# Kernel optimization log

Measured on AMD Instinct MI355X. Metric: run time of the kernel, lower is better.

## Reference

```python
import jax, jax.numpy as jnp
import numpy as np

silu = jax.nn.silu

B, N, E, H, T, L, A = 8, 20000, 40000, 128, 64, 4, 4


def setup_inputs() -> dict:
    key = jax.random.key(0)
    ks = jax.random.split(key, 20)
    s = 0.05
    w = lambda k, shape: jax.random.normal(k, shape, jnp.float32) * s
    return {
        "x": jax.random.normal(ks[0], (B, N, 3), jnp.float32),
        "t": jax.random.uniform(ks[1], (B,), jnp.float32) * 1000.0,
        "atom_types": jax.random.randint(ks[2], (N,), 0, A),
        "bond_indices": jax.random.randint(ks[3], (E, 2), 0, N),
        "emb_table": w(ks[4], (A, H)),
        "W_t1": w(ks[5], (T, H)), "b_t1": jnp.zeros((H,), jnp.float32),
        "W_t2": w(ks[6], (H, H)), "b_t2": jnp.zeros((H,), jnp.float32),
        "W_node": w(ks[7], (H, H)), "b_node": jnp.zeros((H,), jnp.float32),
        "Wm1": w(ks[8], (L, 2 * H + 1, H)), "bm1": jnp.zeros((L, H), jnp.float32),
        "Wm2": w(ks[9], (L, H, H)), "bm2": jnp.zeros((L, H), jnp.float32),
        "Wn1": w(ks[10], (L, 2 * H, H)), "bn1": jnp.zeros((L, H), jnp.float32),
        "Wn2": w(ks[11], (L, H, H)), "bn2": jnp.zeros((L, H), jnp.float32),
        "Wc1": w(ks[12], (L, H, H)), "bc1": jnp.zeros((L, H), jnp.float32),
        "Wc2": w(ks[13], (L, H, 1)) * 0.001,  # xavier gain=0.001 final coord layer
        "W_o1": w(ks[14], (H, H)), "b_o1": jnp.zeros((H,), jnp.float32),
        "W_o2": w(ks[15], (H, 3)), "b_o2": jnp.zeros((3,), jnp.float32),
    }


def reference(x, t, atom_types, bond_indices, emb_table,
              W_t1, b_t1, W_t2, b_t2, W_node, b_node,
              Wm1, bm1, Wm2, bm2, Wn1, bn1, Wn2, bn2, Wc1, bc1, Wc2,
              W_o1, b_o1, W_o2, b_o2):
    n_atoms = x.shape[1]
    src = bond_indices[:, 0]
    dst = bond_indices[:, 1]

    # sinusoidal time embedding -> time MLP
    half = W_t1.shape[0] // 2
    freq = jnp.exp(jnp.arange(half, dtype=jnp.float32) * (-np.log(10000.0) / (half - 1)))
    te = t[:, None] * freq[None, :]
    te = jnp.concatenate([jnp.sin(te), jnp.cos(te)], axis=-1)  # [B, T]
    t_emb = silu(te @ W_t1 + b_t1) @ W_t2 + b_t2  # [B, H]

    # node init: embedding -> linear -> + time emb
    h0 = emb_table[atom_types] @ W_node + b_node  # [N, H]
    h = h0[None, :, :] + t_emb[:, None, :]  # [B, N, H]

    # degree counts (src+dst incidence), clamped to >=1
    ones = jnp.ones((src.shape[0],), jnp.float32)
    counts = jnp.zeros((n_atoms,), jnp.float32).at[dst].add(ones).at[src].add(ones)
    counts = jnp.maximum(counts, 1.0)

    x_orig = x
    n_layers = Wm1.shape[0]
    for l in range(n_layers):
        h_src = h[:, src, :]
        h_dst = h[:, dst, :]
        coord_diff = x[:, dst, :] - x[:, src, :]  # [B, E, 3]
        dist = jnp.sqrt(jnp.sum(coord_diff * coord_diff, axis=-1, keepdims=True))
        msg_in = jnp.concatenate([h_src, h_dst, dist], axis=-1)  # [B, E, 2H+1]
        m = silu(msg_in @ Wm1[l] + bm1[l])
        m = silu(m @ Wm2[l] + bm2[l])  # [B, E, H]

        agg = jnp.zeros_like(h).at[:, dst, :].add(m).at[:, src, :].add(m)
        h_in = jnp.concatenate([h, agg], axis=-1)
        h = h + silu(h_in @ Wn1[l] + bn1[l]) @ Wn2[l] + bn2[l]

        cw = silu(m @ Wc1[l] + bc1[l]) @ Wc2[l]  # [B, E, 1]
        cdn = coord_diff / (dist + 1e-8)
        upd = cdn * cw
        coord_update = jnp.zeros_like(x).at[:, dst, :].add(upd).at[:, src, :].add(-upd)
        x = x + coord_update / counts[None, :, None]

    coord_change = x - x_orig
    noise_from_h = silu(h @ W_o1 + b_o1) @ W_o2 + b_o2
    return coord_change + noise_from_h
```

## Files before the change

### kernel.cpp

```cpp
#include <hip/hip_runtime.h>
#include <math.h>

#define B_ 8
#define N_ 20000
#define E_ 40000
#define H_ 128
#define L_ 4
#define A_ 4
#define TS 132
#define MRS 136
#define EPB 64
#define NPB 64

#define WFENCE __asm__ __volatile__("" ::: "memory")

typedef _Float16 f16x8 __attribute__((ext_vector_type(8)));
typedef _Float16 f16x4v __attribute__((ext_vector_type(4)));
typedef float f32x4 __attribute__((ext_vector_type(4)));

__device__ __forceinline__ float silu_f(float x) {
    return x * __builtin_amdgcn_rcpf(1.f + __expf(-x));
}


__global__ void k_zero(int* __restrict__ deg, int* __restrict__ cursor) {
    int i = blockIdx.x * 256 + threadIdx.x;
    if (i < N_) { deg[i] = 0; cursor[i] = 0; }
}

__global__ void k_deg(const int* __restrict__ bond, int* __restrict__ deg) {
    int e = blockIdx.x * 256 + threadIdx.x;
    if (e < E_) {
        atomicAdd(&deg[bond[2 * e]], 1);
        atomicAdd(&deg[bond[2 * e + 1]], 1);
    }
}

__global__ void k_scan(const int* __restrict__ deg, int* __restrict__ indptr) {
    __shared__ int sums[1024];
    const int CH = (N_ + 1023) / 1024;
    int t = threadIdx.x;
    int s0 = t * CH;
    int s1 = min(s0 + CH, N_);
    int s = 0;
    for (int i = s0; i < s1; ++i) s += deg[i];
    sums[t] = s;
    __syncthreads();
    for (int off = 1; off < 1024; off <<= 1) {
        int v = (t >= off) ? sums[t - off] : 0;
        __syncthreads();
        sums[t] += v;
        __syncthreads();
    }
    int base = (t > 0) ? sums[t - 1] : 0;
    int run = base;
    for (int i = s0; i < s1; ++i) { indptr[i] = run; run += deg[i]; }
    if (s1 == N_ && s0 < N_) indptr[N_] = run;
}

__global__ void k_fill(const int* __restrict__ bond, const int* __restrict__ indptr,
                       int* __restrict__ cursor, int* __restrict__ adj) {
    int e = blockIdx.x * 256 + threadIdx.x;
    if (e < E_) {
        int s = bond[2 * e], d = bond[2 * e + 1];
        int ps = indptr[s] + atomicAdd(&cursor[s], 1);
        adj[ps] = (e << 1);
        int pd = indptr[d] + atomicAdd(&cursor[d], 1);
        adj[pd] = (e << 1) | 1;
    }
}

__global__ void k_wprepL(const float* __restrict__ W, _Float16* __restrict__ Wf,
                         int K, int wstride) {
    int l = blockIdx.y;
    const float* Wl = W + (size_t)l * wstride;
    _Float16* Wfl = Wf + (size_t)l * K * 128;
    int idx = blockIdx.x * 256 + threadIdx.x;
    if (idx >= K * 128) return;
    int j = idx & 7, lane = (idx >> 3) & 63, nt = (idx >> 9) & 7, kt = idx >> 12;
    int k = kt * 32 + (lane >> 4) * 8 + j;
    int n = nt * 16 + (lane & 15);
    Wfl[idx] = (_Float16)Wl[k * 128 + n];
}

__global__ void k_temb(const float* __restrict__ tv,
                       const float* __restrict__ W1, const float* __restrict__ b1,
                       const float* __restrict__ W2, const float* __restrict__ b2,
                       float* __restrict__ t_emb) {
    __shared__ float te[64];
    __shared__ float h1[128];
    int b = blockIdx.x;
    int tid = threadIdx.x;
    float tval = tv[b];
    if (tid < 32) {
        float fr = __expf((float)tid * (-logf(10000.f) / 31.f));
        float a = tval * fr;
        te[tid] = sinf(a);
        te[tid + 32] = cosf(a);
    }
    __syncthreads();
    float acc = b1[tid];
    for (int k = 0; k < 64; ++k) acc += te[k] * W1[k * 128 + tid];
    h1[tid] = silu_f(acc);
    __syncthreads();
    float acc2 = b2[tid];
    for (int k = 0; k < 128; ++k) acc2 += h1[k] * W2[k * 128 + tid];
    t_emb[b * 128 + tid] = acc2;
}

__global__ void k_embproj(const float* __restrict__ emb, const float* __restrict__ W,
                          const float* __restrict__ bias, float* __restrict__ outp) {
    int tid = threadIdx.x;
    int a = tid >> 7, j = tid & 127;
    float acc = bias[j];
    for (int k = 0; k < 128; ++k) acc += emb[a * 128 + k] * W[k * 128 + j];
    outp[a * 128 + j] = acc;
}

__global__ void k_hinit(const int* __restrict__ at, const float* __restrict__ embp,
                        const float* __restrict__ temb, float* __restrict__ h,
                        _Float16* __restrict__ h16) {
    size_t idx4 = (size_t)blockIdx.x * 256 + threadIdx.x;
    size_t e0 = idx4 * 4;
    int j = (int)(e0 % H_);
    size_t bn = e0 / H_;
    int n = (int)(bn % N_);
    int b = (int)(bn / N_);
    int a = at[n];
    float4 ep = *(const float4*)(embp + a * H_ + j);
    float4 tv = *(const float4*)(temb + b * H_ + j);
    float4 r = make_float4(ep.x + tv.x, ep.y + tv.y, ep.z + tv.z, ep.w + tv.w);
    ((float4*)h)[idx4] = r;
    f16x4v o;
    o[0] = (_Float16)r.x; o[1] = (_Float16)r.y; o[2] = (_Float16)r.z; o[3] = (_Float16)r.w;
    *(f16x4v*)(h16 + e0) = o;
}

__global__ void k_xcopy(const float* __restrict__ x, float* __restrict__ xb) {
    int i = blockIdx.x * 256 + threadIdx.x;
    xb[i] = x[i];
}

template <int RS, int KT>
__device__ __forceinline__ void mfma_gemm(const _Float16* Asw, const _Float16* __restrict__ Wf,
                                          f32x4 (&acc)[8], int ml, int quad, int lane) {
    #pragma unroll
    for (int kt = 0; kt < KT; ++kt) {
        f16x8 a = *(const f16x8*)(Asw + ml * RS + kt * 32 + quad * 8);
        #pragma unroll
        for (int nt = 0; nt < 8; ++nt) {
            f16x8 b = *(const f16x8*)(Wf + (((kt * 8 + nt) * 64 + lane) * 8));
            acc[nt] = __builtin_amdgcn_mfma_f32_16x16x32_f16(a, b, acc[nt], 0, 0, 0);
        }
    }
}

template <int RS, int KT>
__device__ __forceinline__ void mfma_gemm2(const _Float16* Asw, const _Float16* __restrict__ Wf,
                                           f32x4 (&acc)[2][8], int ml, int quad, int lane) {
    #pragma unroll
    for (int kt = 0; kt < KT; ++kt) {
        f16x8 a0 = *(const f16x8*)(Asw + ml * RS + kt * 32 + quad * 8);
        f16x8 a1 = *(const f16x8*)(Asw + (16 + ml) * RS + kt * 32 + quad * 8);
        #pragma unroll
        for (int nt = 0; nt < 8; ++nt) {
            f16x8 b = *(const f16x8*)(Wf + (((kt * 8 + nt) * 64 + lane) * 8));
            acc[0][nt] = __builtin_amdgcn_mfma_f32_16x16x32_f16(a0, b, acc[0][nt], 0, 0, 0);
            acc[1][nt] = __builtin_amdgcn_mfma_f32_16x16x32_f16(a1, b, acc[1][nt], 0, 0, 0);
        }
    }
}

template <int STRIDE, int K>
__device__ __forceinline__ void gemm_t(const float* As, const float* __restrict__ W,
                                       float (&acc)[4][8], int r4, int c) {
    const float4* Wv = (const float4*)W;
    #pragma unroll 2
    for (int k = 0; k < K; k += 4) {
        float a[4][4];
        #pragma unroll
        for (int i = 0; i < 4; ++i)
            *(float4*)a[i] = *(const float4*)(As + (r4 + i) * STRIDE + k);
        #pragma unroll
        for (int kk = 0; kk < 4; ++kk) {
            float4 w0 = Wv[(k + kk) * 32 + c * 2];
            float4 w1 = Wv[(k + kk) * 32 + c * 2 + 1];
            #pragma unroll
            for (int i = 0; i < 4; ++i) {
                float av = a[i][kk];
                acc[i][0] += av * w0.x; acc[i][1] += av * w0.y;
                acc[i][2] += av * w0.z; acc[i][3] += av * w0.w;
                acc[i][4] += av * w1.x; acc[i][5] += av * w1.y;
                acc[i][6] += av * w1.z; acc[i][7] += av * w1.w;
            }
        }
    }
}

__device__ __forceinline__ void bias_init(float (&acc)[4][8], const float* __restrict__ bias, int c) {
    float4 b0 = ((const float4*)bias)[c * 2];
    float4 b1 = ((const float4*)bias)[c * 2 + 1];
    #pragma unroll
    for (int i = 0; i < 4; ++i) {
        acc[i][0] = b0.x; acc[i][1] = b0.y; acc[i][2] = b0.z; acc[i][3] = b0.w;
        acc[i][4] = b1.x; acc[i][5] = b1.y; acc[i][6] = b1.z; acc[i][7] = b1.w;
    }
}


__global__ __launch_bounds__(128, 4) void k_edge_mfma(
    const _Float16* __restrict__ h16, const float* __restrict__ xcur,
    const int* __restrict__ bond,
    const float* __restrict__ Wm1, const float* __restrict__ bm1,
    const _Float16* __restrict__ Wm1f,
    const float* __restrict__ bm2, const _Float16* __restrict__ Wm2f,
    const float* __restrict__ bc1, const _Float16* __restrict__ Wc1f,
    const float* __restrict__ Wc2,
    _Float16* __restrict__ m16, float* __restrict__ cw_out) {
    __shared__ _Float16 As[EPB * MRS];
    __shared__ float ds_s[EPB];
    int tid = threadIdx.x;
    int b = blockIdx.x & 7;
    int e0 = (blockIdx.x >> 3) * EPB;
    size_t be0 = (size_t)b * E_ + e0;

    int el = tid >> 1, q = tid & 1;
    int2 sd = ((const int2*)bond)[e0 + el];
    int s = sd.x, d = sd.y;
    if (q == 0) {
        const float* xs = xcur + ((size_t)b * N_ + s) * 3;
        const float* xd = xcur + ((size_t)b * N_ + d) * 3;
        float dx = xd[0] - xs[0], dy = xd[1] - xs[1], dz = xd[2] - xs[2];
        ds_s[el] = sqrtf(dx * dx + dy * dy + dz * dz);
    }
    {
        const _Float16* hs = h16 + ((size_t)b * N_ + s) * H_;
        #pragma unroll
        for (int j = 0; j < 8; ++j)
            *(f16x8*)(As + el * MRS + q * 64 + j * 8) = *(const f16x8*)(hs + q * 64 + j * 8);
    }
    WFENCE;

    int lane = tid & 63, w = tid >> 6;
    int ml = lane & 15, quad = lane >> 4;
    _Float16* Asw = As + w * 32 * MRS;
    const float* wd = Wm1 + 256 * H_;

    f32x4 acc[2][8];
    #pragma unroll
    for (int nt = 0; nt < 8; ++nt) {
        int col = nt * 16 + ml;
        float bb = bm1[col];
        float ww = wd[col];
        #pragma unroll
        for (int rt = 0; rt < 2; ++rt)
            #pragma unroll
            for (int r = 0; r < 4; ++r)
                acc[rt][nt][r] = bb + ds_s[w * 32 + rt * 16 + quad * 4 + r] * ww;
    }
    mfma_gemm2<MRS, 4>(Asw, Wm1f, acc, ml, quad, lane);
    WFENCE;
    {
        const _Float16* hd = h16 + ((size_t)b * N_ + d) * H_;
        #pragma unroll
        for (int j = 0; j < 8; ++j)
            *(f16x8*)(As + el * MRS + q * 64 + j * 8) = *(const f16x8*)(hd + q * 64 + j * 8);
    }
    WFENCE;
    mfma_gemm2<MRS, 4>(Asw, Wm1f + 4 * 8 * 64 * 8, acc, ml, quad, lane);
    WFENCE;
    #pragma unroll
    for (int rt = 0; rt < 2; ++rt)
        #pragma unroll
        for (int nt = 0; nt < 8; ++nt)
            #pragma unroll
            for (int r = 0; r < 4; ++r)
                Asw[(rt * 16 + quad * 4 + r) * MRS + nt * 16 + ml] = (_Float16)silu_f(acc[rt][nt][r]);
    WFENCE;

    #pragma unroll
    for (int nt = 0; nt < 8; ++nt) {
        float bb = bm2[nt * 16 + ml];
        #pragma unroll
        for (int rt = 0; rt < 2; ++rt)
            #pragma unroll
            for (int r = 0; r < 4; ++r) acc[rt][nt][r] = bb;
    }
    mfma_gemm2<MRS, 4>(Asw, Wm2f, acc, ml, quad, lane);
    WFENCE;
    #pragma unroll
    for (int rt = 0; rt < 2; ++rt)
        #pragma unroll
        for (int nt = 0; nt < 8; ++nt)
            #pragma unroll
            for (int r = 0; r < 4; ++r)
                Asw[(rt * 16 + quad * 4 + r) * MRS + nt * 16 + ml] = (_Float16)silu_f(acc[rt][nt][r]);
    WFENCE;
    #pragma unroll
    for (int j = 0; j < 8; ++j)
        *(f16x8*)(m16 + (be0 + el) * H_ + q * 64 + j * 8) =
            *(const f16x8*)(As + el * MRS + q * 64 + j * 8);

    #pragma unroll
    for (int nt = 0; nt < 8; ++nt) {
        float bb = bc1[nt * 16 + ml];
        #pragma unroll
        for (int rt = 0; rt < 2; ++rt)
            #pragma unroll
            for (int r = 0; r < 4; ++r) acc[rt][nt][r] = bb;
    }
    mfma_gemm2<MRS, 4>(Asw, Wc1f, acc, ml, quad, lane);
    float part[2][4] = {{0.f, 0.f, 0.f, 0.f}, {0.f, 0.f, 0.f, 0.f}};
    #pragma unroll
    for (int nt = 0; nt < 8; ++nt) {
        float wv = Wc2[nt * 16 + ml];
        #pragma unroll
        for (int rt = 0; rt < 2; ++rt)
            #pragma unroll
            for (int r = 0; r < 4; ++r) part[rt][r] += silu_f(acc[rt][nt][r]) * wv;
    }
    #pragma unroll
    for (int off = 1; off < 16; off <<= 1)
        #pragma unroll
        for (int rt = 0; rt < 2; ++rt)
            #pragma unroll
            for (int r = 0; r < 4; ++r) part[rt][r] += __shfl_xor(part[rt][r], off, 64);
    if (ml == 0) {
        #pragma unroll
        for (int rt = 0; rt < 2; ++rt)
            #pragma unroll
            for (int r = 0; r < 4; ++r)
                cw_out[be0 + w * 32 + rt * 16 + quad * 4 + r] = part[rt][r];
    }
}

__global__ void k_coord(const float* __restrict__ xcur, float* __restrict__ xnext,
                        const float* __restrict__ cw, const int* __restrict__ bond,
                        const int* __restrict__ indptr, const int* __restrict__ adj) {
    int idx = blockIdx.x * 256 + threadIdx.x;
    int b = idx / N_;
    int n = idx - b * N_;
    const float* xb = xcur + (size_t)b * N_ * 3;
    int p0 = indptr[n], p1 = indptr[n + 1];
    float ax = 0.f, ay = 0.f, az = 0.f;
    for (int p = p0; p < p1; ++p) {
        int a = adj[p];
        int e = a >> 1;
        float sgn = (a & 1) ? 1.f : -1.f;
        int s = bond[2 * e], d = bond[2 * e + 1];
        float dx = xb[d * 3 + 0] - xb[s * 3 + 0];
        float dy = xb[d * 3 + 1] - xb[s * 3 + 1];
        float dz = xb[d * 3 + 2] - xb[s * 3 + 2];
        float dist = sqrtf(dx * dx + dy * dy + dz * dz);
        float w = cw[(size_t)b * E_ + e] * sgn * __builtin_amdgcn_rcpf(dist + 1e-8f);
        ax += dx * w; ay += dy * w; az += dz * w;
    }
    float rcnt = __builtin_amdgcn_rcpf((float)max(p1 - p0, 1));
    xnext[(size_t)idx * 3 + 0] = xb[n * 3 + 0] + ax * rcnt;
    xnext[(size_t)idx * 3 + 1] = xb[n * 3 + 1] + ay * rcnt;
    xnext[(size_t)idx * 3 + 2] = xb[n * 3 + 2] + az * rcnt;
}

__global__ __launch_bounds__(256, 5) void k_node_mfma(
    float* __restrict__ h, _Float16* __restrict__ h16,
    const _Float16* __restrict__ m16,
    const int* __restrict__ indptr, const int* __restrict__ adj,
    const float* __restrict__ bn1, const _Float16* __restrict__ Wn1f,
    const float* __restrict__ bn2, const _Float16* __restrict__ Wn2f) {
    __shared__ _Float16 As[NPB * MRS];
    int tid = threadIdx.x;
    int el = tid >> 2, q = tid & 3;
    int be = blockIdx.x * NPB + el;
    int b = be / N_, n = be - b * N_;
    {
        const _Float16* hr = h16 + (size_t)be * H_;
        #pragma unroll
        for (int j = 0; j < 4; ++j)
            *(f16x8*)(As + el * MRS + q * 32 + j * 8) = *(const f16x8*)(hr + q * 32 + j * 8);
    }
    WFENCE;

    int lane = tid & 63, w = tid >> 6;
    int ml = lane & 15, quad = lane >> 4;
    _Float16* Asw = As + w * 16 * MRS;
    size_t be0 = (size_t)blockIdx.x * NPB;

    f32x4 acc[8];
    #pragma unroll
    for (int nt = 0; nt < 8; ++nt) {
        float bb = bn1[nt * 16 + ml];
        #pragma unroll
        for (int r = 0; r < 4; ++r) acc[nt][r] = bb;
    }
    mfma_gemm<MRS, 4>(Asw, Wn1f, acc, ml, quad, lane);
    WFENCE;
    {
        float ag[4][8];
        #pragma unroll
        for (int j = 0; j < 4; ++j)
            #pragma unroll
            for (int i = 0; i < 8; ++i) ag[j][i] = 0.f;
        int p0 = indptr[n], p1 = indptr[n + 1];
        for (int p = p0; p < p1; ++p) {
            int e = adj[p] >> 1;
            const _Float16* mp = m16 + ((size_t)b * E_ + e) * H_;
            #pragma unroll
            for (int j = 0; j < 4; ++j) {
                f16x8 v = *(const f16x8*)(mp + q * 32 + j * 8);
                #pragma unroll
                for (int i = 0; i < 8; ++i) ag[j][i] += (float)v[i];
            }
        }
        #pragma unroll
        for (int j = 0; j < 4; ++j) {
            f16x8 o;
            #pragma unroll
            for (int i = 0; i < 8; ++i) o[i] = (_Float16)ag[j][i];
            *(f16x8*)(As + el * MRS + q * 32 + j * 8) = o;
        }
    }
    WFENCE;
    mfma_gemm<MRS, 4>(Asw, Wn1f + 4 * 8 * 64 * 8, acc, ml, quad, lane);
    WFENCE;
    #pragma unroll
    for (int nt = 0; nt < 8; ++nt)
        #pragma unroll
        for (int r = 0; r < 4; ++r)
            Asw[(quad * 4 + r) * MRS + nt * 16 + ml] = (_Float16)silu_f(acc[nt][r]);
    WFENCE;
    f32x4 acc2[8];
    #pragma unroll
    for (int nt = 0; nt < 8; ++nt) {
        float bb = bn2[nt * 16 + ml];
        #pragma unroll
        for (int r = 0; r < 4; ++r) acc2[nt][r] = bb;
    }
    mfma_gemm<MRS, 4>(Asw, Wn2f, acc2, ml, quad, lane);
    #pragma unroll
    for (int nt = 0; nt < 8; ++nt)
        #pragma unroll
        for (int r = 0; r < 4; ++r) {
            int row = w * 16 + quad * 4 + r;
            size_t g = (size_t)(be0 + row) * H_ + nt * 16 + ml;
            float v = h[g] + acc2[nt][r];
            h[g] = v;
            h16[g] = (_Float16)v;
        }
}

__global__ __launch_bounds__(256) void k_out2(
    const float* __restrict__ h, const float* __restrict__ xfin, const float* __restrict__ xorig,
    const float* __restrict__ Wo1, const float* __restrict__ bo1,
    const float* __restrict__ Wo2, const float* __restrict__ bo2,
    float* __restrict__ out) {
    __shared__ float As[64 * TS];
    __shared__ float red[64 * 48];
    int tid = threadIdx.x;
    {
        int nl = tid >> 2, q = tid & 3;
        size_t row = (size_t)blockIdx.x * 64 + nl;
        const float4* hr = (const float4*)(h + row * H_);
        #pragma unroll
        for (int j = 0; j < 8; ++j) {
            int f4 = j * 4 + q;
            *(float4*)(As + nl * TS + f4 * 4) = hr[f4];
        }
    }
    __syncthreads();
    int r4 = (tid >> 4) * 4, c = tid & 15;
    float acc[4][8];
    bias_init(acc, bo1, c);
    gemm_t<TS, 128>(As, Wo1, acc, r4, c);
    #pragma unroll
    for (int i = 0; i < 4; ++i) {
        float p0 = 0.f, p1 = 0.f, p2 = 0.f;
        #pragma unroll
        for (int j = 0; j < 8; ++j) {
            float u = silu_f(acc[i][j]);
            int col = c * 8 + j;
            p0 += u * Wo2[col * 3 + 0];
            p1 += u * Wo2[col * 3 + 1];
            p2 += u * Wo2[col * 3 + 2];
        }
        red[(r4 + i) * 48 + c * 3 + 0] = p0;
        red[(r4 + i) * 48 + c * 3 + 1] = p1;
        red[(r4 + i) * 48 + c * 3 + 2] = p2;
    }
    __syncthreads();
    if (tid < 192) {
        int row = tid / 3, jj = tid - row * 3;
        float s = 0.f;
        #pragma unroll
        for (int cc = 0; cc < 16; ++cc) s += red[row * 48 + cc * 3 + jj];
        size_t grow = (size_t)blockIdx.x * 64 + row;
        out[grow * 3 + jj] = s + bo2[jj] + xfin[grow * 3 + jj] - xorig[grow * 3 + jj];
    }
}


extern "C" void kernel_launch(void* const* d_in, const int* in_sizes, int n_in,
                              void* d_out, int out_size, void* d_ws, size_t ws_size,
                              hipStream_t stream) {
    const float* x = (const float*)d_in[0];
    const float* t = (const float*)d_in[1];
    const int* atom_types = (const int*)d_in[2];
    const int* bond = (const int*)d_in[3];
    const float* emb_table = (const float*)d_in[4];
    const float* W_t1 = (const float*)d_in[5];
    const float* b_t1 = (const float*)d_in[6];
    const float* W_t2 = (const float*)d_in[7];
    const float* b_t2 = (const float*)d_in[8];
    const float* W_node = (const float*)d_in[9];
    const float* b_node = (const float*)d_in[10];
    const float* Wm1 = (const float*)d_in[11];
    const float* bm1 = (const float*)d_in[12];
    const float* Wm2 = (const float*)d_in[13];
    const float* bm2 = (const float*)d_in[14];
    const float* Wn1 = (const float*)d_in[15];
    const float* bn1 = (const float*)d_in[16];
    const float* Wn2 = (const float*)d_in[17];
    const float* bn2 = (const float*)d_in[18];
    const float* Wc1 = (const float*)d_in[19];
    const float* bc1 = (const float*)d_in[20];
    const float* Wc2 = (const float*)d_in[21];
    const float* W_o1 = (const float*)d_in[22];
    const float* b_o1 = (const float*)d_in[23];
    const float* W_o2 = (const float*)d_in[24];
    const float* b_o2 = (const float*)d_in[25];
    float* out = (float*)d_out;

    char* p = (char*)d_ws;
    auto alloc = [&](size_t bytes) -> void* {
        void* r = (void*)p;
        p += (bytes + 255) & ~(size_t)255;
        return r;
    };
    float* t_emb = (float*)alloc((size_t)B_ * H_ * 4);
    float* emb_proj = (float*)alloc((size_t)A_ * H_ * 4);
    int* deg = (int*)alloc((size_t)N_ * 4);
    int* indptr = (int*)alloc((size_t)(N_ + 1) * 4);
    int* cursor = (int*)alloc((size_t)N_ * 4);
    int* adj = (int*)alloc((size_t)2 * E_ * 4);
    float* xb0 = (float*)alloc((size_t)B_ * N_ * 3 * 4);
    float* xb1 = (float*)alloc((size_t)B_ * N_ * 3 * 4);
    float* cw = (float*)alloc((size_t)B_ * E_ * 4);
    float* h = (float*)alloc((size_t)B_ * N_ * H_ * 4);
    _Float16* h16 = (_Float16*)alloc((size_t)B_ * N_ * H_ * 2);
    _Float16* m16 = (_Float16*)alloc((size_t)B_ * E_ * H_ * 2);
    _Float16* Wm1f = (_Float16*)alloc((size_t)L_ * 256 * H_ * 2);
    _Float16* Wm2f = (_Float16*)alloc((size_t)L_ * H_ * H_ * 2);
    _Float16* Wc1f = (_Float16*)alloc((size_t)L_ * H_ * H_ * 2);
    _Float16* Wn1f = (_Float16*)alloc((size_t)L_ * 256 * H_ * 2);
    _Float16* Wn2f = (_Float16*)alloc((size_t)L_ * H_ * H_ * 2);

    k_zero<<<(N_ + 255) / 256, 256, 0, stream>>>(deg, cursor);
    k_deg<<<(E_ + 255) / 256, 256, 0, stream>>>(bond, deg);
    k_scan<<<1, 1024, 0, stream>>>(deg, indptr);
    k_fill<<<(E_ + 255) / 256, 256, 0, stream>>>(bond, indptr, cursor, adj);
    k_temb<<<B_, 128, 0, stream>>>(t, W_t1, b_t1, W_t2, b_t2, t_emb);
    k_embproj<<<1, 512, 0, stream>>>(emb_table, W_node, b_node, emb_proj);
    k_hinit<<<(B_ * N_ * H_ / 4) / 256, 256, 0, stream>>>(atom_types, emb_proj, t_emb, h, h16);
    k_xcopy<<<(B_ * N_ * 3) / 256, 256, 0, stream>>>(x, xb0);
    k_wprepL<<<dim3(128, L_), 256, 0, stream>>>(Wm1, Wm1f, 256, 257 * H_);
    k_wprepL<<<dim3(64, L_), 256, 0, stream>>>(Wm2, Wm2f, 128, H_ * H_);
    k_wprepL<<<dim3(64, L_), 256, 0, stream>>>(Wc1, Wc1f, 128, H_ * H_);
    k_wprepL<<<dim3(128, L_), 256, 0, stream>>>(Wn1, Wn1f, 256, 2 * H_ * H_);
    k_wprepL<<<dim3(64, L_), 256, 0, stream>>>(Wn2, Wn2f, 128, H_ * H_);

    float* xc = xb0;
    float* xn = xb1;
    for (int l = 0; l < L_; ++l) {
        k_edge_mfma<<<(B_ * E_) / EPB, 128, 0, stream>>>(
            h16, xc, bond,
            Wm1 + (size_t)l * 257 * H_, bm1 + l * H_, Wm1f + (size_t)l * 256 * H_,
            bm2 + l * H_, Wm2f + (size_t)l * H_ * H_,
            bc1 + l * H_, Wc1f + (size_t)l * H_ * H_,
            Wc2 + (size_t)l * H_, m16, cw);
        k_coord<<<(B_ * N_) / 256, 256, 0, stream>>>(xc, xn, cw, bond, indptr, adj);
        k_node_mfma<<<(B_ * N_) / NPB, 256, 0, stream>>>(
            h, h16, m16, indptr, adj,
            bn1 + l * H_, Wn1f + (size_t)l * 256 * H_,
            bn2 + l * H_, Wn2f + (size_t)l * H_ * H_);
        float* tmp = xc; xc = xn; xn = tmp;
    }
    k_out2<<<(B_ * N_) / 64, 256, 0, stream>>>(h, xc, x, W_o1, b_o1, W_o2, b_o2, out);
}
```

Measured before the change: 1.129 ms.

## Use four waves per edge block and prefetch src/dst rows into registers

The edge kernel now runs 256 threads per 64-edge block, so each wave handles 16 edge rows instead of 32 and holds half the accumulator registers (single-tile mfma_gemm instead of mfma_gemm2). Launch bounds rise to 256 threads with 5 blocks per CU to raise occupancy. Both the source and destination h rows are loaded into registers at kernel start, so the destination gather latency overlaps the first GEMM instead of stalling between the two halves. In exchange, each weight tile is reloaded by twice as many waves per edge, which adds weight-read traffic.

```diff
diff --git a/kernel.cpp b/kernel.cpp
--- a/kernel.cpp
+++ b/kernel.cpp
@@ -208,7 +208,7 @@
 }
 
 
-__global__ __launch_bounds__(128, 4) void k_edge_mfma(
+__global__ __launch_bounds__(256, 5) void k_edge_mfma(
     const _Float16* __restrict__ h16, const float* __restrict__ xcur,
     const int* __restrict__ bond,
     const float* __restrict__ Wm1, const float* __restrict__ bm1,
@@ -224,9 +224,20 @@
     int e0 = (blockIdx.x >> 3) * EPB;
     size_t be0 = (size_t)b * E_ + e0;
 
-    int el = tid >> 1, q = tid & 1;
+    int el = tid >> 2, q = tid & 3;
     int2 sd = ((const int2*)bond)[e0 + el];
     int s = sd.x, d = sd.y;
+
+    const _Float16* hs = h16 + ((size_t)b * N_ + s) * H_ + q * 32;
+    f16x8 ps0 = *(const f16x8*)(hs);
+    f16x8 ps1 = *(const f16x8*)(hs + 8);
+    f16x8 ps2 = *(const f16x8*)(hs + 16);
+    f16x8 ps3 = *(const f16x8*)(hs + 24);
+    const _Float16* hd = h16 + ((size_t)b * N_ + d) * H_ + q * 32;
+    f16x8 pd0 = *(const f16x8*)(hd);
+    f16x8 pd1 = *(const f16x8*)(hd + 8);
+    f16x8 pd2 = *(const f16x8*)(hd + 16);
+    f16x8 pd3 = *(const f16x8*)(hd + 24);
     if (q == 0) {
         const float* xs = xcur + ((size_t)b * N_ + s) * 3;
         const float* xd = xcur + ((size_t)b * N_ + d) * 3;
@@ -234,103 +245,87 @@
         ds_s[el] = sqrtf(dx * dx + dy * dy + dz * dz);
     }
     {
-        const _Float16* hs = h16 + ((size_t)b * N_ + s) * H_;
-        #pragma unroll
-        for (int j = 0; j < 8; ++j)
-            *(f16x8*)(As + el * MRS + q * 64 + j * 8) = *(const f16x8*)(hs + q * 64 + j * 8);
+        _Float16* ap = As + el * MRS + q * 32;
+        *(f16x8*)(ap) = ps0; *(f16x8*)(ap + 8) = ps1;
+        *(f16x8*)(ap + 16) = ps2; *(f16x8*)(ap + 24) = ps3;
     }
     WFENCE;
 
     int lane = tid & 63, w = tid >> 6;
     int ml = lane & 15, quad = lane >> 4;
-    _Float16* Asw = As + w * 32 * MRS;
+    _Float16* Asw = As + w * 16 * MRS;
     const float* wd = Wm1 + 256 * H_;
 
-    f32x4 acc[2][8];
+    float dl[4];
+    #pragma unroll
+    for (int r = 0; r < 4; ++r) dl[r] = ds_s[w * 16 + quad * 4 + r];
+    f32x4 acc[8];
     #pragma unroll
     for (int nt = 0; nt < 8; ++nt) {
         int col = nt * 16 + ml;
         float bb = bm1[col];
         float ww = wd[col];
         #pragma unroll
-        for (int rt = 0; rt < 2; ++rt)
-            #pragma unroll
-            for (int r = 0; r < 4; ++r)
-                acc[rt][nt][r] = bb + ds_s[w * 32 + rt * 16 + quad * 4 + r] * ww;
-    }
-    mfma_gemm2<MRS, 4>(Asw, Wm1f, acc, ml, quad, lane);
+        for (int r = 0; r < 4; ++r) acc[nt][r] = bb + dl[r] * ww;
+    }
+    mfma_gemm<MRS, 4>(Asw, Wm1f, acc, ml, quad, lane);
     WFENCE;
     {
-        const _Float16* hd = h16 + ((size_t)b * N_ + d) * H_;
-        #pragma unroll
-        for (int j = 0; j < 8; ++j)
-            *(f16x8*)(As + el * MRS + q * 64 + j * 8) = *(const f16x8*)(hd + q * 64 + j * 8);
-    }
-    WFENCE;
-    mfma_gemm2<MRS, 4>(Asw, Wm1f + 4 * 8 * 64 * 8, acc, ml, quad, lane);
-    WFENCE;
-    #pragma unroll
-    for (int rt = 0; rt < 2; ++rt)
-        #pragma unroll
-        for (int nt = 0; nt < 8; ++nt)
-            #pragma unroll
-            for (int r = 0; r < 4; ++r)
-                Asw[(rt * 16 + quad * 4 + r) * MRS + nt * 16 + ml] = (_Float16)silu_f(acc[rt][nt][r]);
+        _Float16* ap = As + el * MRS + q * 32;
+        *(f16x8*)(ap) = pd0; *(f16x8*)(ap + 8) = pd1;
+        *(f16x8*)(ap + 16) = pd2; *(f16x8*)(ap + 24) = pd3;
+    }
+    WFENCE;
+    mfma_gemm<MRS, 4>(Asw, Wm1f + 4 * 8 * 64 * 8, acc, ml, quad, lane);
+    WFENCE;
+    #pragma unroll
+    for (int nt = 0; nt < 8; ++nt)
+        #pragma unroll
+        for (int r = 0; r < 4; ++r)
+            Asw[(quad * 4 + r) * MRS + nt * 16 + ml] = (_Float16)silu_f(acc[nt][r]);
     WFENCE;
 
     #pragma unroll
     for (int nt = 0; nt < 8; ++nt) {
         float bb = bm2[nt * 16 + ml];
         #pragma unroll
-        for (int rt = 0; rt < 2; ++rt)
-            #pragma unroll
-            for (int r = 0; r < 4; ++r) acc[rt][nt][r] = bb;
-    }
-    mfma_gemm2<MRS, 4>(Asw, Wm2f, acc, ml, quad, lane);
-    WFENCE;
-    #pragma unroll
-    for (int rt = 0; rt < 2; ++rt)
-        #pragma unroll
-        for (int nt = 0; nt < 8; ++nt)
-            #pragma unroll
-            for (int r = 0; r < 4; ++r)
-                Asw[(rt * 16 + quad * 4 + r) * MRS + nt * 16 + ml] = (_Float16)silu_f(acc[rt][nt][r]);
-    WFENCE;
-    #pragma unroll
-    for (int j = 0; j < 8; ++j)
-        *(f16x8*)(m16 + (be0 + el) * H_ + q * 64 + j * 8) =
-            *(const f16x8*)(As + el * MRS + q * 64 + j * 8);
+        for (int r = 0; r < 4; ++r) acc[nt][r] = bb;
+    }
+    mfma_gemm<MRS, 4>(Asw, Wm2f, acc, ml, quad, lane);
+    WFENCE;
+    #pragma unroll
+    for (int nt = 0; nt < 8; ++nt)
+        #pragma unroll
+        for (int r = 0; r < 4; ++r)
+            Asw[(quad * 4 + r) * MRS + nt * 16 + ml] = (_Float16)silu_f(acc[nt][r]);
+    WFENCE;
+    #pragma unroll
+    for (int j = 0; j < 4; ++j)
+        *(f16x8*)(m16 + (be0 + el) * H_ + q * 32 + j * 8) =
+            *(const f16x8*)(As + el * MRS + q * 32 + j * 8);
 
     #pragma unroll
     for (int nt = 0; nt < 8; ++nt) {
         float bb = bc1[nt * 16 + ml];
         #pragma unroll
-        for (int rt = 0; rt < 2; ++rt)
-            #pragma unroll
-            for (int r = 0; r < 4; ++r) acc[rt][nt][r] = bb;
-    }
-    mfma_gemm2<MRS, 4>(Asw, Wc1f, acc, ml, quad, lane);
-    float part[2][4] = {{0.f, 0.f, 0.f, 0.f}, {0.f, 0.f, 0.f, 0.f}};
+        for (int r = 0; r < 4; ++r) acc[nt][r] = bb;
+    }
+    mfma_gemm<MRS, 4>(Asw, Wc1f, acc, ml, quad, lane);
+    float part[4] = {0.f, 0.f, 0.f, 0.f};
     #pragma unroll
     for (int nt = 0; nt < 8; ++nt) {
         float wv = Wc2[nt * 16 + ml];
         #pragma unroll
-        for (int rt = 0; rt < 2; ++rt)
-            #pragma unroll
-            for (int r = 0; r < 4; ++r) part[rt][r] += silu_f(acc[rt][nt][r]) * wv;
+        for (int r = 0; r < 4; ++r) part[r] += silu_f(acc[nt][r]) * wv;
     }
     #pragma unroll
     for (int off = 1; off < 16; off <<= 1)
         #pragma unroll
-        for (int rt = 0; rt < 2; ++rt)
-            #pragma unroll
-            for (int r = 0; r < 4; ++r) part[rt][r] += __shfl_xor(part[rt][r], off, 64);
+        for (int r = 0; r < 4; ++r) part[r] += __shfl_xor(part[r], off, 64);
     if (ml == 0) {
         #pragma unroll
-        for (int rt = 0; rt < 2; ++rt)
-            #pragma unroll
-            for (int r = 0; r < 4; ++r)
-                cw_out[be0 + w * 32 + rt * 16 + quad * 4 + r] = part[rt][r];
+        for (int r = 0; r < 4; ++r)
+            cw_out[be0 + w * 16 + quad * 4 + r] = part[r];
     }
 }
 
@@ -570,7 +565,7 @@
     float* xc = xb0;
     float* xn = xb1;
     for (int l = 0; l < L_; ++l) {
-        k_edge_mfma<<<(B_ * E_) / EPB, 128, 0, stream>>>(
+        k_edge_mfma<<<(B_ * E_) / EPB, 256, 0, stream>>>(
             h16, xc, bond,
             Wm1 + (size_t)l * 257 * H_, bm1 + l * H_, Wm1f + (size_t)l * 256 * H_,
             bm2 + l * H_, Wm2f + (size_t)l * H_ * H_,
```

Measured after the change: 1.148 ms. No clear change (+1.6%).

## Double tile size, prefetch weight fragments, and swizzle blocks across XCDs

Applied to the files above, without the earlier changes.

Edge and node kernels now process 128 rows per block with 256 threads, and each wave computes two 16-row MFMA tiles so every weight fragment load is reused twice. A new GEMM helper double-buffers the B-operand weight fragments in registers, loading k-step kt+1 while the MFMAs for step kt run. Block indices are remapped so consecutive tiles land on the same XCD, which should improve L2 locality, and the edge kernel now overlaps the gather loads with the distance computation. The larger register footprint lowers the occupancy hint and could limit latency hiding.

```diff
diff --git a/kernel.cpp b/kernel.cpp
--- a/kernel.cpp
+++ b/kernel.cpp
@@ -9,8 +9,8 @@
 #define A_ 4
 #define TS 132
 #define MRS 136
-#define EPB 64
-#define NPB 64
+#define EPB 128
+#define NPB 128
 
 #define WFENCE __asm__ __volatile__("" ::: "memory")
 
@@ -20,6 +20,12 @@
 
 __device__ __forceinline__ float silu_f(float x) {
     return x * __builtin_amdgcn_rcpf(1.f + __expf(-x));
+}
+
+__device__ __forceinline__ int xcd_swz(int bid, int nwg) {
+    int q = nwg >> 3, r = nwg & 7;
+    int x = bid & 7, i = bid >> 3;
+    return (x < r ? x * (q + 1) : r * (q + 1) + (x - r) * q) + i;
 }
 
 
@@ -141,32 +147,26 @@
     xb[i] = x[i];
 }
 
-template <int RS, int KT>
-__device__ __forceinline__ void mfma_gemm(const _Float16* Asw, const _Float16* __restrict__ Wf,
-                                          f32x4 (&acc)[8], int ml, int quad, int lane) {
-    #pragma unroll
-    for (int kt = 0; kt < KT; ++kt) {
-        f16x8 a = *(const f16x8*)(Asw + ml * RS + kt * 32 + quad * 8);
-        #pragma unroll
-        for (int nt = 0; nt < 8; ++nt) {
-            f16x8 b = *(const f16x8*)(Wf + (((kt * 8 + nt) * 64 + lane) * 8));
-            acc[nt] = __builtin_amdgcn_mfma_f32_16x16x32_f16(a, b, acc[nt], 0, 0, 0);
-        }
-    }
-}
-
-template <int RS, int KT>
-__device__ __forceinline__ void mfma_gemm2(const _Float16* Asw, const _Float16* __restrict__ Wf,
-                                           f32x4 (&acc)[2][8], int ml, int quad, int lane) {
-    #pragma unroll
-    for (int kt = 0; kt < KT; ++kt) {
+template <int RS>
+__device__ __forceinline__ void mfma_gemm2p(const _Float16* Asw, const _Float16* __restrict__ Wf,
+                                            f32x4 (&acc)[2][8], int ml, int quad, int lane) {
+    const _Float16* wp = Wf + lane * 8;
+    f16x8 bb[2][8];
+    #pragma unroll
+    for (int nt = 0; nt < 8; ++nt) bb[0][nt] = *(const f16x8*)(wp + nt * 512);
+    #pragma unroll
+    for (int kt = 0; kt < 4; ++kt) {
+        if (kt < 3) {
+            #pragma unroll
+            for (int nt = 0; nt < 8; ++nt)
+                bb[(kt + 1) & 1][nt] = *(const f16x8*)(wp + ((kt + 1) * 8 + nt) * 512);
+        }
         f16x8 a0 = *(const f16x8*)(Asw + ml * RS + kt * 32 + quad * 8);
         f16x8 a1 = *(const f16x8*)(Asw + (16 + ml) * RS + kt * 32 + quad * 8);
         #pragma unroll
         for (int nt = 0; nt < 8; ++nt) {
-            f16x8 b = *(const f16x8*)(Wf + (((kt * 8 + nt) * 64 + lane) * 8));
-            acc[0][nt] = __builtin_amdgcn_mfma_f32_16x16x32_f16(a0, b, acc[0][nt], 0, 0, 0);
-            acc[1][nt] = __builtin_amdgcn_mfma_f32_16x16x32_f16(a1, b, acc[1][nt], 0, 0, 0);
+            acc[0][nt] = __builtin_amdgcn_mfma_f32_16x16x32_f16(a0, bb[kt & 1][nt], acc[0][nt], 0, 0, 0);
+            acc[1][nt] = __builtin_amdgcn_mfma_f32_16x16x32_f16(a1, bb[kt & 1][nt], acc[1][nt], 0, 0, 0);
         }
     }
 }
@@ -208,7 +208,7 @@
 }
 
 
-__global__ __launch_bounds__(128, 4) void k_edge_mfma(
+__global__ __launch_bounds__(256, 3) void k_edge_mfma(
     const _Float16* __restrict__ h16, const float* __restrict__ xcur,
     const int* __restrict__ bond,
     const float* __restrict__ Wm1, const float* __restrict__ bm1,
@@ -220,54 +220,63 @@
     __shared__ _Float16 As[EPB * MRS];
     __shared__ float ds_s[EPB];
     int tid = threadIdx.x;
-    int b = blockIdx.x & 7;
-    int e0 = (blockIdx.x >> 3) * EPB;
-    size_t be0 = (size_t)b * E_ + e0;
+    int sbid = xcd_swz(blockIdx.x, (B_ * E_) / EPB);
+    size_t base = (size_t)sbid * EPB;
 
     int el = tid >> 1, q = tid & 1;
-    int2 sd = ((const int2*)bond)[e0 + el];
+    int gei = sbid * EPB + el;
+    int b = gei / E_;
+    int e = gei - b * E_;
+    int2 sd = ((const int2*)bond)[e];
     int s = sd.x, d = sd.y;
-    if (q == 0) {
-        const float* xs = xcur + ((size_t)b * N_ + s) * 3;
-        const float* xd = xcur + ((size_t)b * N_ + d) * 3;
-        float dx = xd[0] - xs[0], dy = xd[1] - xs[1], dz = xd[2] - xs[2];
-        ds_s[el] = sqrtf(dx * dx + dy * dy + dz * dz);
-    }
+
     {
-        const _Float16* hs = h16 + ((size_t)b * N_ + s) * H_;
-        #pragma unroll
-        for (int j = 0; j < 8; ++j)
-            *(f16x8*)(As + el * MRS + q * 64 + j * 8) = *(const f16x8*)(hs + q * 64 + j * 8);
+        const _Float16* hs = h16 + ((size_t)b * N_ + s) * H_ + q * 64;
+        f16x8 ps[8];
+        #pragma unroll
+        for (int j = 0; j < 8; ++j) ps[j] = *(const f16x8*)(hs + j * 8);
+        if (q == 0) {
+            const float* xs = xcur + ((size_t)b * N_ + s) * 3;
+            const float* xd = xcur + ((size_t)b * N_ + d) * 3;
+            float dx = xd[0] - xs[0], dy = xd[1] - xs[1], dz = xd[2] - xs[2];
+            ds_s[el] = sqrtf(dx * dx + dy * dy + dz * dz);
+        }
+        _Float16* ap = As + el * MRS + q * 64;
+        #pragma unroll
+        for (int j = 0; j < 8; ++j) *(f16x8*)(ap + j * 8) = ps[j];
     }
     WFENCE;
 
     int lane = tid & 63, w = tid >> 6;
     int ml = lane & 15, quad = lane >> 4;
     _Float16* Asw = As + w * 32 * MRS;
-    const float* wd = Wm1 + 256 * H_;
+    const float* wdist = Wm1 + 256 * H_;
 
     f32x4 acc[2][8];
     #pragma unroll
     for (int nt = 0; nt < 8; ++nt) {
         int col = nt * 16 + ml;
         float bb = bm1[col];
-        float ww = wd[col];
+        float ww = wdist[col];
         #pragma unroll
         for (int rt = 0; rt < 2; ++rt)
             #pragma unroll
             for (int r = 0; r < 4; ++r)
                 acc[rt][nt][r] = bb + ds_s[w * 32 + rt * 16 + quad * 4 + r] * ww;
     }
-    mfma_gemm2<MRS, 4>(Asw, Wm1f, acc, ml, quad, lane);
+    mfma_gemm2p<MRS>(Asw, Wm1f, acc, ml, quad, lane);
     WFENCE;
     {
-        const _Float16* hd = h16 + ((size_t)b * N_ + d) * H_;
-        #pragma unroll
-        for (int j = 0; j < 8; ++j)
-            *(f16x8*)(As + el * MRS + q * 64 + j * 8) = *(const f16x8*)(hd + q * 64 + j * 8);
-    }
-    WFENCE;
-    mfma_gemm2<MRS, 4>(Asw, Wm1f + 4 * 8 * 64 * 8, acc, ml, quad, lane);
+        const _Float16* hd = h16 + ((size_t)b * N_ + d) * H_ + q * 64;
+        f16x8 pd[8];
+        #pragma unroll
+        for (int j = 0; j < 8; ++j) pd[j] = *(const f16x8*)(hd + j * 8);
+        _Float16* ap = As + el * MRS + q * 64;
+        #pragma unroll
+        for (int j = 0; j < 8; ++j) *(f16x8*)(ap + j * 8) = pd[j];
+    }
+    WFENCE;
+    mfma_gemm2p<MRS>(Asw, Wm1f + 4 * 8 * 64 * 8, acc, ml, quad, lane);
     WFENCE;
     #pragma unroll
     for (int rt = 0; rt < 2; ++rt)
@@ -286,7 +295,7 @@
             #pragma unroll
             for (int r = 0; r < 4; ++r) acc[rt][nt][r] = bb;
     }
-    mfma_gemm2<MRS, 4>(Asw, Wm2f, acc, ml, quad, lane);
+    mfma_gemm2p<MRS>(Asw, Wm2f, acc, ml, quad, lane);
     WFENCE;
     #pragma unroll
     for (int rt = 0; rt < 2; ++rt)
@@ -298,7 +307,7 @@
     WFENCE;
     #pragma unroll
     for (int j = 0; j < 8; ++j)
-        *(f16x8*)(m16 + (be0 + el) * H_ + q * 64 + j * 8) =
+        *(f16x8*)(m16 + (size_t)gei * H_ + q * 64 + j * 8) =
             *(const f16x8*)(As + el * MRS + q * 64 + j * 8);
 
     #pragma unroll
@@ -309,7 +318,7 @@
             #pragma unroll
             for (int r = 0; r < 4; ++r) acc[rt][nt][r] = bb;
     }
-    mfma_gemm2<MRS, 4>(Asw, Wc1f, acc, ml, quad, lane);
+    mfma_gemm2p<MRS>(Asw, Wc1f, acc, ml, quad, lane);
     float part[2][4] = {{0.f, 0.f, 0.f, 0.f}, {0.f, 0.f, 0.f, 0.f}};
     #pragma unroll
     for (int nt = 0; nt < 8; ++nt) {
@@ -330,7 +339,7 @@
         for (int rt = 0; rt < 2; ++rt)
             #pragma unroll
             for (int r = 0; r < 4; ++r)
-                cw_out[be0 + w * 32 + rt * 16 + quad * 4 + r] = part[rt][r];
+                cw_out[base + w * 32 + rt * 16 + quad * 4 + r] = part[rt][r];
     }
 }
 
@@ -361,7 +370,7 @@
     xnext[(size_t)idx * 3 + 2] = xb[n * 3 + 2] + az * rcnt;
 }
 
-__global__ __launch_bounds__(256, 5) void k_node_mfma(
+__global__ __launch_bounds__(256, 3) void k_node_mfma(
     float* __restrict__ h, _Float16* __restrict__ h16,
     const _Float16* __restrict__ m16,
     const int* __restrict__ indptr, const int* __restrict__ adj,
@@ -369,83 +378,92 @@
     const float* __restrict__ bn2, const _Float16* __restrict__ Wn2f) {
     __shared__ _Float16 As[NPB * MRS];
     int tid = threadIdx.x;
-    int el = tid >> 2, q = tid & 3;
-    int be = blockIdx.x * NPB + el;
+    int sbid = xcd_swz(blockIdx.x, (B_ * N_) / NPB);
+    int el = tid >> 1, q = tid & 1;
+    int be = sbid * NPB + el;
     int b = be / N_, n = be - b * N_;
     {
-        const _Float16* hr = h16 + (size_t)be * H_;
-        #pragma unroll
-        for (int j = 0; j < 4; ++j)
-            *(f16x8*)(As + el * MRS + q * 32 + j * 8) = *(const f16x8*)(hr + q * 32 + j * 8);
+        const _Float16* hr = h16 + (size_t)be * H_ + q * 64;
+        #pragma unroll
+        for (int j = 0; j < 8; ++j)
+            *(f16x8*)(As + el * MRS + q * 64 + j * 8) = *(const f16x8*)(hr + j * 8);
     }
     WFENCE;
 
     int lane = tid & 63, w = tid >> 6;
     int ml = lane & 15, quad = lane >> 4;
-    _Float16* Asw = As + w * 16 * MRS;
-    size_t be0 = (size_t)blockIdx.x * NPB;
-
-    f32x4 acc[8];
+    _Float16* Asw = As + w * 32 * MRS;
+    size_t be0 = (size_t)sbid * NPB;
+
+    f32x4 acc[2][8];
     #pragma unroll
     for (int nt = 0; nt < 8; ++nt) {
         float bb = bn1[nt * 16 + ml];
         #pragma unroll
-        for (int r = 0; r < 4; ++r) acc[nt][r] = bb;
-    }
-    mfma_gemm<MRS, 4>(Asw, Wn1f, acc, ml, quad, lane);
+        for (int rt = 0; rt < 2; ++rt)
+            #pragma unroll
+            for (int r = 0; r < 4; ++r) acc[rt][nt][r] = bb;
+    }
+    mfma_gemm2p<MRS>(Asw, Wn1f, acc, ml, quad, lane);
     WFENCE;
     {
-        float ag[4][8];
-        #pragma unroll
-        for (int j = 0; j < 4; ++j)
+        float ag[8][8];
+        #pragma unroll
+        for (int j = 0; j < 8; ++j)
             #pragma unroll
             for (int i = 0; i < 8; ++i) ag[j][i] = 0.f;
         int p0 = indptr[n], p1 = indptr[n + 1];
         for (int p = p0; p < p1; ++p) {
             int e = adj[p] >> 1;
-            const _Float16* mp = m16 + ((size_t)b * E_ + e) * H_;
-            #pragma unroll
-            for (int j = 0; j < 4; ++j) {
-                f16x8 v = *(const f16x8*)(mp + q * 32 + j * 8);
+            const _Float16* mp = m16 + ((size_t)b * E_ + e) * H_ + q * 64;
+            #pragma unroll
+            for (int j = 0; j < 8; ++j) {
+                f16x8 v = *(const f16x8*)(mp + j * 8);
                 #pragma unroll
                 for (int i = 0; i < 8; ++i) ag[j][i] += (float)v[i];
             }
         }
         #pragma unroll
-        for (int j = 0; j < 4; ++j) {
+        for (int j = 0; j < 8; ++j) {
             f16x8 o;
             #pragma unroll
             for (int i = 0; i < 8; ++i) o[i] = (_Float16)ag[j][i];
-            *(f16x8*)(As + el * MRS + q * 32 + j * 8) = o;
-        }
-    }
-    WFENCE;
-    mfma_gemm<MRS, 4>(Asw, Wn1f + 4 * 8 * 64 * 8, acc, ml, quad, lane);
-    WFENCE;
-    #pragma unroll
-    for (int nt = 0; nt < 8; ++nt)
-        #pragma unroll
-        for (int r = 0; r < 4; ++r)
-            Asw[(quad * 4 + r) * MRS + nt * 16 + ml] = (_Float16)silu_f(acc[nt][r]);
-    WFENCE;
-    f32x4 acc2[8];
+            *(f16x8*)(As + el * MRS + q * 64 + j * 8) = o;
+        }
+    }
+    WFENCE;
+    mfma_gemm2p<MRS>(Asw, Wn1f + 4 * 8 * 64 * 8, acc, ml, quad, lane);
+    WFENCE;
+    #pragma unroll
+    for (int rt = 0; rt < 2; ++rt)
+        #pragma unroll
+        for (int nt = 0; nt < 8; ++nt)
+            #pragma unroll
+            for (int r = 0; r < 4; ++r)
+                Asw[(rt * 16 + quad * 4 + r) * MRS + nt * 16 + ml] = (_Float16)silu_f(acc[rt][nt][r]);
+    WFENCE;
+    f32x4 acc2[2][8];
     #pragma unroll
     for (int nt = 0; nt < 8; ++nt) {
         float bb = bn2[nt * 16 + ml];
         #pragma unroll
-        for (int r = 0; r < 4; ++r) acc2[nt][r] = bb;
-    }
-    mfma_gemm<MRS, 4>(Asw, Wn2f, acc2, ml, quad, lane);
-    #pragma unroll
-    for (int nt = 0; nt < 8; ++nt)
-        #pragma unroll
-        for (int r = 0; r < 4; ++r) {
-            int row = w * 16 + quad * 4 + r;
-            size_t g = (size_t)(be0 + row) * H_ + nt * 16 + ml;
-            float v = h[g] + acc2[nt][r];
-            h[g] = v;
-            h16[g] = (_Float16)v;
-        }
+        for (int rt = 0; rt < 2; ++rt)
+            #pragma unroll
+            for (int r = 0; r < 4; ++r) acc2[rt][nt][r] = bb;
+    }
+    mfma_gemm2p<MRS>(Asw, Wn2f, acc2, ml, quad, lane);
+    #pragma unroll
+    for (int rt = 0; rt < 2; ++rt)
+        #pragma unroll
+        for (int nt = 0; nt < 8; ++nt)
+            #pragma unroll
+            for (int r = 0; r < 4; ++r) {
+                int row = w * 32 + rt * 16 + quad * 4 + r;
+                size_t g = (size_t)(be0 + row) * H_ + nt * 16 + ml;
+                float v = h[g] + acc2[rt][nt][r];
+                h[g] = v;
+                h16[g] = (_Float16)v;
+            }
 }
 
 __global__ __launch_bounds__(256) void k_out2(
@@ -570,7 +588,7 @@
     float* xc = xb0;
     float* xn = xb1;
     for (int l = 0; l < L_; ++l) {
-        k_edge_mfma<<<(B_ * E_) / EPB, 128, 0, stream>>>(
+        k_edge_mfma<<<(B_ * E_) / EPB, 256, 0, stream>>>(
             h16, xc, bond,
             Wm1 + (size_t)l * 257 * H_, bm1 + l * H_, Wm1f + (size_t)l * 256 * H_,
             bm2 + l * H_, Wm2f + (size_t)l * H_ * H_,
```

After: 1.410 ms. 1.25x slower.

## Prefetch edge gathers into registers and give node-kernel waves two row tiles

Applied to the files above, without the earlier changes.

The edge kernel now loads both the source and destination h16 rows into registers at the start, so the destination gather is in flight while the first MFMA pass runs. Its occupancy hint drops from 4 to 3 to make room for the extra registers. The node kernel goes from 256 to 128 threads per block, with each wave computing 32 rows through the two-tile MFMA helper so every weight fragment is reused twice. Its message aggregation runs in two halves to keep register use down. The cost is fewer resident waves per CU and less latency hiding in the node kernel.

```diff
diff --git a/kernel.cpp b/kernel.cpp
--- a/kernel.cpp
+++ b/kernel.cpp
@@ -142,20 +142,6 @@
 }
 
 template <int RS, int KT>
-__device__ __forceinline__ void mfma_gemm(const _Float16* Asw, const _Float16* __restrict__ Wf,
-                                          f32x4 (&acc)[8], int ml, int quad, int lane) {
-    #pragma unroll
-    for (int kt = 0; kt < KT; ++kt) {
-        f16x8 a = *(const f16x8*)(Asw + ml * RS + kt * 32 + quad * 8);
-        #pragma unroll
-        for (int nt = 0; nt < 8; ++nt) {
-            f16x8 b = *(const f16x8*)(Wf + (((kt * 8 + nt) * 64 + lane) * 8));
-            acc[nt] = __builtin_amdgcn_mfma_f32_16x16x32_f16(a, b, acc[nt], 0, 0, 0);
-        }
-    }
-}
-
-template <int RS, int KT>
 __device__ __forceinline__ void mfma_gemm2(const _Float16* Asw, const _Float16* __restrict__ Wf,
                                            f32x4 (&acc)[2][8], int ml, int quad, int lane) {
     #pragma unroll
@@ -208,7 +194,7 @@
 }
 
 
-__global__ __launch_bounds__(128, 4) void k_edge_mfma(
+__global__ __launch_bounds__(128, 3) void k_edge_mfma(
     const _Float16* __restrict__ h16, const float* __restrict__ xcur,
     const int* __restrict__ bond,
     const float* __restrict__ Wm1, const float* __restrict__ bm1,
@@ -227,6 +213,14 @@
     int el = tid >> 1, q = tid & 1;
     int2 sd = ((const int2*)bond)[e0 + el];
     int s = sd.x, d = sd.y;
+
+    const _Float16* hs = h16 + ((size_t)b * N_ + s) * H_ + q * 64;
+    const _Float16* hd = h16 + ((size_t)b * N_ + d) * H_ + q * 64;
+    f16x8 ps[8], pd[8];
+    #pragma unroll
+    for (int j = 0; j < 8; ++j) ps[j] = *(const f16x8*)(hs + j * 8);
+    #pragma unroll
+    for (int j = 0; j < 8; ++j) pd[j] = *(const f16x8*)(hd + j * 8);
     if (q == 0) {
         const float* xs = xcur + ((size_t)b * N_ + s) * 3;
         const float* xd = xcur + ((size_t)b * N_ + d) * 3;
@@ -234,10 +228,9 @@
         ds_s[el] = sqrtf(dx * dx + dy * dy + dz * dz);
     }
     {
-        const _Float16* hs = h16 + ((size_t)b * N_ + s) * H_;
-        #pragma unroll
-        for (int j = 0; j < 8; ++j)
-            *(f16x8*)(As + el * MRS + q * 64 + j * 8) = *(const f16x8*)(hs + q * 64 + j * 8);
+        _Float16* ap = As + el * MRS + q * 64;
+        #pragma unroll
+        for (int j = 0; j < 8; ++j) *(f16x8*)(ap + j * 8) = ps[j];
     }
     WFENCE;
 
@@ -261,10 +254,9 @@
     mfma_gemm2<MRS, 4>(Asw, Wm1f, acc, ml, quad, lane);
     WFENCE;
     {
-        const _Float16* hd = h16 + ((size_t)b * N_ + d) * H_;
-        #pragma unroll
-        for (int j = 0; j < 8; ++j)
-            *(f16x8*)(As + el * MRS + q * 64 + j * 8) = *(const f16x8*)(hd + q * 64 + j * 8);
+        _Float16* ap = As + el * MRS + q * 64;
+        #pragma unroll
+        for (int j = 0; j < 8; ++j) *(f16x8*)(ap + j * 8) = pd[j];
     }
     WFENCE;
     mfma_gemm2<MRS, 4>(Asw, Wm1f + 4 * 8 * 64 * 8, acc, ml, quad, lane);
@@ -361,7 +353,7 @@
     xnext[(size_t)idx * 3 + 2] = xb[n * 3 + 2] + az * rcnt;
 }
 
-__global__ __launch_bounds__(256, 5) void k_node_mfma(
+__global__ __launch_bounds__(128, 3) void k_node_mfma(
     float* __restrict__ h, _Float16* __restrict__ h16,
     const _Float16* __restrict__ m16,
     const int* __restrict__ indptr, const int* __restrict__ adj,
@@ -369,83 +361,93 @@
     const float* __restrict__ bn2, const _Float16* __restrict__ Wn2f) {
     __shared__ _Float16 As[NPB * MRS];
     int tid = threadIdx.x;
-    int el = tid >> 2, q = tid & 3;
+    int el = tid >> 1, q = tid & 1;
     int be = blockIdx.x * NPB + el;
     int b = be / N_, n = be - b * N_;
     {
-        const _Float16* hr = h16 + (size_t)be * H_;
-        #pragma unroll
-        for (int j = 0; j < 4; ++j)
-            *(f16x8*)(As + el * MRS + q * 32 + j * 8) = *(const f16x8*)(hr + q * 32 + j * 8);
+        const _Float16* hr = h16 + (size_t)be * H_ + q * 64;
+        #pragma unroll
+        for (int j = 0; j < 8; ++j)
+            *(f16x8*)(As + el * MRS + q * 64 + j * 8) = *(const f16x8*)(hr + j * 8);
     }
     WFENCE;
 
     int lane = tid & 63, w = tid >> 6;
     int ml = lane & 15, quad = lane >> 4;
-    _Float16* Asw = As + w * 16 * MRS;
+    _Float16* Asw = As + w * 32 * MRS;
     size_t be0 = (size_t)blockIdx.x * NPB;
 
-    f32x4 acc[8];
+    f32x4 acc[2][8];
     #pragma unroll
     for (int nt = 0; nt < 8; ++nt) {
         float bb = bn1[nt * 16 + ml];
         #pragma unroll
-        for (int r = 0; r < 4; ++r) acc[nt][r] = bb;
-    }
-    mfma_gemm<MRS, 4>(Asw, Wn1f, acc, ml, quad, lane);
+        for (int rt = 0; rt < 2; ++rt)
+            #pragma unroll
+            for (int r = 0; r < 4; ++r) acc[rt][nt][r] = bb;
+    }
+    mfma_gemm2<MRS, 4>(Asw, Wn1f, acc, ml, quad, lane);
     WFENCE;
     {
-        float ag[4][8];
-        #pragma unroll
-        for (int j = 0; j < 4; ++j)
-            #pragma unroll
-            for (int i = 0; i < 8; ++i) ag[j][i] = 0.f;
         int p0 = indptr[n], p1 = indptr[n + 1];
-        for (int p = p0; p < p1; ++p) {
-            int e = adj[p] >> 1;
-            const _Float16* mp = m16 + ((size_t)b * E_ + e) * H_;
+        #pragma unroll 1
+        for (int half = 0; half < 2; ++half) {
+            float ag[4][8];
+            #pragma unroll
+            for (int j = 0; j < 4; ++j)
+                #pragma unroll
+                for (int i = 0; i < 8; ++i) ag[j][i] = 0.f;
+            for (int p = p0; p < p1; ++p) {
+                int e = adj[p] >> 1;
+                const _Float16* mp = m16 + ((size_t)b * E_ + e) * H_ + q * 64 + half * 32;
+                #pragma unroll
+                for (int j = 0; j < 4; ++j) {
+                    f16x8 v = *(const f16x8*)(mp + j * 8);
+                    #pragma unroll
+                    for (int i = 0; i < 8; ++i) ag[j][i] += (float)v[i];
+                }
+            }
             #pragma unroll
             for (int j = 0; j < 4; ++j) {
-                f16x8 v = *(const f16x8*)(mp + q * 32 + j * 8);
+                f16x8 o;
                 #pragma unroll
-                for (int i = 0; i < 8; ++i) ag[j][i] += (float)v[i];
+                for (int i = 0; i < 8; ++i) o[i] = (_Float16)ag[j][i];
+                *(f16x8*)(As + el * MRS + q * 64 + half * 32 + j * 8) = o;
             }
         }
-        #pragma unroll
-        for (int j = 0; j < 4; ++j) {
-            f16x8 o;
-            #pragma unroll
-            for (int i = 0; i < 8; ++i) o[i] = (_Float16)ag[j][i];
-            *(f16x8*)(As + el * MRS + q * 32 + j * 8) = o;
-        }
-    }
-    WFENCE;
-    mfma_gemm<MRS, 4>(Asw, Wn1f + 4 * 8 * 64 * 8, acc, ml, quad, lane);
-    WFENCE;
-    #pragma unroll
-    for (int nt = 0; nt < 8; ++nt)
-        #pragma unroll
-        for (int r = 0; r < 4; ++r)
-            Asw[(quad * 4 + r) * MRS + nt * 16 + ml] = (_Float16)silu_f(acc[nt][r]);
-    WFENCE;
-    f32x4 acc2[8];
+    }
+    WFENCE;
+    mfma_gemm2<MRS, 4>(Asw, Wn1f + 4 * 8 * 64 * 8, acc, ml, quad, lane);
+    WFENCE;
+    #pragma unroll
+    for (int rt = 0; rt < 2; ++rt)
+        #pragma unroll
+        for (int nt = 0; nt < 8; ++nt)
+            #pragma unroll
+            for (int r = 0; r < 4; ++r)
+                Asw[(rt * 16 + quad * 4 + r) * MRS + nt * 16 + ml] = (_Float16)silu_f(acc[rt][nt][r]);
+    WFENCE;
     #pragma unroll
     for (int nt = 0; nt < 8; ++nt) {
         float bb = bn2[nt * 16 + ml];
         #pragma unroll
-        for (int r = 0; r < 4; ++r) acc2[nt][r] = bb;
-    }
-    mfma_gemm<MRS, 4>(Asw, Wn2f, acc2, ml, quad, lane);
-    #pragma unroll
-    for (int nt = 0; nt < 8; ++nt)
-        #pragma unroll
-        for (int r = 0; r < 4; ++r) {
-            int row = w * 16 + quad * 4 + r;
-            size_t g = (size_t)(be0 + row) * H_ + nt * 16 + ml;
-            float v = h[g] + acc2[nt][r];
-            h[g] = v;
-            h16[g] = (_Float16)v;
-        }
+        for (int rt = 0; rt < 2; ++rt)
+            #pragma unroll
+            for (int r = 0; r < 4; ++r) acc[rt][nt][r] = bb;
+    }
+    mfma_gemm2<MRS, 4>(Asw, Wn2f, acc, ml, quad, lane);
+    #pragma unroll
+    for (int rt = 0; rt < 2; ++rt)
+        #pragma unroll
+        for (int nt = 0; nt < 8; ++nt)
+            #pragma unroll
+            for (int r = 0; r < 4; ++r) {
+                int row = w * 32 + rt * 16 + quad * 4 + r;
+                size_t g = (size_t)(be0 + row) * H_ + nt * 16 + ml;
+                float v = h[g] + acc[rt][nt][r];
+                h[g] = v;
+                h16[g] = (_Float16)v;
+            }
 }
 
 __global__ __launch_bounds__(256) void k_out2(
@@ -577,7 +579,7 @@
             bc1 + l * H_, Wc1f + (size_t)l * H_ * H_,
             Wc2 + (size_t)l * H_, m16, cw);
         k_coord<<<(B_ * N_) / 256, 256, 0, stream>>>(xc, xn, cw, bond, indptr, adj);
-        k_node_mfma<<<(B_ * N_) / NPB, 256, 0, stream>>>(
+        k_node_mfma<<<(B_ * N_) / NPB, 128, 0, stream>>>(
             h, h16, m16, indptr, adj,
             bn1 + l * H_, Wn1f + (size_t)l * 256 * H_,
             bn2 + l * H_, Wn2f + (size_t)l * H_ * H_);
```

Measured after the change: 1.240 ms. 1.1x slower.
